# Kernel optimization log

Hardware: AMD Instinct MI355X
Metric: run time of the kernel (lower is better)

The kernel has to match this reference:

```python
import jax, jax.numpy as jnp
import numpy as np

B, S, E, H = 4, 2048, 1024, 16
DH = E // H
EXP = 1024  # FeedForwardPart default expansion_dim
EPS = 1e-5


def layer_norm(x, gamma, beta):
    mu = jnp.mean(x, axis=-1, keepdims=True)
    var = jnp.var(x, axis=-1, keepdims=True)
    return (x - mu) * jax.lax.rsqrt(var + EPS) * gamma + beta


def setup_inputs() -> dict:
    key = jax.random.key(0)
    ks = jax.random.split(key, 8)
    s = 0.02
    return {
        "x": jax.random.normal(ks[0], (B, S, E), jnp.float32),
        "mask": jnp.ones((B, 1, 1, S), jnp.int32),
        "wq": jax.random.normal(ks[1], (E, E), jnp.float32) * s,
        "wk": jax.random.normal(ks[2], (E, E), jnp.float32) * s,
        "wv": jax.random.normal(ks[3], (E, E), jnp.float32) * s,
        "wo": jax.random.normal(ks[4], (E, E), jnp.float32) * s,
        "bo": jnp.zeros((E,), jnp.float32),
        "w1": jax.random.normal(ks[5], (E, EXP), jnp.float32) * s,
        "b1": jnp.zeros((EXP,), jnp.float32),
        "w2": jax.random.normal(ks[6], (EXP, E), jnp.float32) * s,
        "b2": jnp.zeros((E,), jnp.float32),
        "gamma": jnp.ones((E,), jnp.float32),
        "beta": jnp.zeros((E,), jnp.float32),
    }


def reference(x, mask, wq, wk, wv, wo, bo, w1, b1, w2, b2, gamma, beta):
    # Multi-head self-attention
    q = (x @ wq).reshape(B, S, H, DH)
    k = (x @ wk).reshape(B, S, H, DH)
    v = (x @ wv).reshape(B, S, H, DH)
    scores = jnp.einsum("bqhd,bkhd->bhqk", q, k) / jnp.sqrt(jnp.float32(DH))
    scores = jnp.where(mask == 0, jnp.float32(-1e10), scores)
    attn = jax.nn.softmax(scores, axis=-1)
    ctx = jnp.einsum("bhqk,bkhd->bqhd", attn, v).reshape(B, S, E)
    attn_out = ctx @ wo + bo
    # Residual + shared LayerNorm
    h = layer_norm(attn_out + x, gamma, beta)
    # FFN (expansion 1024 per source default)
    ff = jax.nn.relu(h @ w1 + b1) @ w2 + b2
    return layer_norm(ff + h, gamma, beta)
```

## Files before the change

### kernel.cpp

```cpp
#include <hip/hip_runtime.h>
#include <hip/hip_bf16.h>

typedef short s16x8 __attribute__((ext_vector_type(8)));
typedef float f32x4 __attribute__((ext_vector_type(4)));
typedef float f32x16 __attribute__((ext_vector_type(16)));
typedef unsigned short u16;

#define B_ 4
#define S_ 2048
#define E_ 1024
#define H_ 16
#define DH_ 64

__device__ __forceinline__ u16 f2b(float f) {
  union { float f; unsigned u; } x; x.f = f;
  unsigned r = (x.u + 0x7fffu + ((x.u >> 16) & 1u)) >> 16;
  return (u16)r;
}

__device__ __forceinline__ float b2f(u16 v) {
  union { unsigned u; float f; } x; x.u = ((unsigned)v) << 16; return x.f;
}

__device__ __forceinline__ unsigned pk2(float lo, float hi) {
  __hip_bfloat162 h = __float22bfloat162_rn(float2{lo, hi});
  union { __hip_bfloat162 h; unsigned u; } c; c.h = h; return c.u;
}

__device__ __forceinline__ void xsw(unsigned& x, unsigned& y, int hi) {
  unsigned s = hi ? x : y;
  unsigned r = (unsigned)__shfl_xor((int)s, 32);
  unsigned nx = hi ? r : x;
  unsigned ny = hi ? y : r;
  x = nx; y = ny;
}

__device__ __forceinline__ void async16(const void* g, void* l) {
  __builtin_amdgcn_global_load_lds((const __attribute__((address_space(1))) void*)g,
                                   (__attribute__((address_space(3))) void*)l,
                                   16, 0, 0);
}

__global__ __launch_bounds__(256) void k_cast(const float* __restrict__ in,
                                              u16* __restrict__ out, int n4) {
  int i = blockIdx.x * 256 + threadIdx.x;
  if (i >= n4) return;
  float4 v = ((const float4*)in)[i];
  ushort4 o;
  o.x = f2b(v.x); o.y = f2b(v.y); o.z = f2b(v.z); o.w = f2b(v.w);
  ((ushort4*)out)[i] = o;
}

__global__ __launch_bounds__(256) void k_castT(const float* __restrict__ in,
                                               u16* __restrict__ out, int K, int N) {
  __shared__ float tile[32][33];
  int k0 = blockIdx.x * 32, n0 = blockIdx.y * 32;
  int tx = threadIdx.x, ty = threadIdx.y;
#pragma unroll
  for (int i = 0; i < 32; i += 8)
    tile[ty + i][tx] = in[(long)(k0 + ty + i) * N + n0 + tx];
  __syncthreads();
#pragma unroll
  for (int i = 0; i < 32; i += 8)
    out[(long)(n0 + ty + i) * K + k0 + tx] = f2b(tile[tx][ty + i]);
}

__global__ __launch_bounds__(256, 2) void k_gemm(
    const u16* __restrict__ A, const u16* __restrict__ Bt,
    int N, int K,
    const float* __restrict__ bias, int relu, int mode,
    float* __restrict__ outF, u16* __restrict__ outB,
    u16* __restrict__ oq, u16* __restrict__ ok, u16* __restrict__ ov) {
  __shared__ __align__(16) u16 Al[128 * 32];
  __shared__ __align__(16) u16 Bl[128 * 32];
  const int t = threadIdx.x;
  const int lane = t & 63, w = t >> 6;
  const int g = lane >> 4, li = lane & 15;
  const int wr = w >> 1, wc = w & 1;
  const int bm = blockIdx.x * 128, bn = blockIdx.y * 128;

  f32x4 acc[4][4] = {};

  const long ar0 = bm + (t >> 2), ar1 = bm + ((256 + t) >> 2);
  const long br0 = bn + (t >> 2), br1 = bn + ((256 + t) >> 2);
  const int c0 = (t & 3) * 8, c1 = ((256 + t) & 3) * 8;
  u16* aD0 = &Al[(w * 64) * 8];
  u16* aD1 = &Al[(256 + w * 64) * 8];
  u16* bD0 = &Bl[(w * 64) * 8];
  u16* bD1 = &Bl[(256 + w * 64) * 8];

  for (int kt = 0; kt < K; kt += 32) {
    async16(&A[ar0 * K + kt + c0], aD0);
    async16(&A[ar1 * K + kt + c1], aD1);
    async16(&Bt[br0 * K + kt + c0], bD0);
    async16(&Bt[br1 * K + kt + c1], bD1);
    __syncthreads();
    s16x8 af[4], bf[4];
#pragma unroll
    for (int mi = 0; mi < 4; ++mi)
      af[mi] = *(const s16x8*)&Al[(wr * 64 + mi * 16 + li) * 32 + g * 8];
#pragma unroll
    for (int nf = 0; nf < 4; ++nf)
      bf[nf] = *(const s16x8*)&Bl[(wc * 64 + nf * 16 + li) * 32 + g * 8];
#pragma unroll
    for (int mi = 0; mi < 4; ++mi)
#pragma unroll
      for (int nf = 0; nf < 4; ++nf)
        acc[mi][nf] = __builtin_amdgcn_mfma_f32_16x16x32_bf16(af[mi], bf[nf], acc[mi][nf], 0, 0, 0);
    __syncthreads();
  }

#pragma unroll
  for (int mi = 0; mi < 4; ++mi)
#pragma unroll
    for (int nf = 0; nf < 4; ++nf) {
      int col = bn + wc * 64 + nf * 16 + li;
      if (mode == 1) {
        int which = col >> 10, cc = col & 1023;
        int hh = cc >> 6, dd = cc & 63;
        u16* dst = which == 0 ? oq : (which == 1 ? ok : ov);
        float scl = which == 0 ? 0.125f : 1.f;
#pragma unroll
        for (int r = 0; r < 4; ++r) {
          long row = bm + wr * 64 + mi * 16 + g * 4 + r;
          int b2 = (int)(row >> 11), ss = (int)(row & 2047);
          dst[(((long)b2 * H_ + hh) * S_ + ss) * DH_ + dd] = f2b(acc[mi][nf][r] * scl);
        }
      } else {
        float bv = bias ? bias[col] : 0.f;
#pragma unroll
        for (int r = 0; r < 4; ++r) {
          long row = bm + wr * 64 + mi * 16 + g * 4 + r;
          float v = acc[mi][nf][r] + bv;
          if (relu) v = fmaxf(v, 0.f);
          if (outF) outF[row * N + col] = v;
          if (outB) outB[row * N + col] = f2b(v);
        }
      }
    }
}

__global__ __launch_bounds__(512, 1) void k_attn(
    const u16* __restrict__ Q, const u16* __restrict__ Kg, const u16* __restrict__ Vg,
    const int* __restrict__ mask, u16* __restrict__ ctx) {
  __shared__ __align__(16) u16 Kl[3][64 * 64];
  __shared__ __align__(16) u16 Vt[3][64 * 72];
  __shared__ __align__(16) float MBs[S_];
  __shared__ __align__(16) float BC[8 * 32];
  const int t = threadIdx.x;
  const int lane = t & 63, wid = t >> 6;
  const int q = lane & 31, hi = lane >> 5;
  const int bh = blockIdx.x;
  const int b = bh >> 4, h = bh & 15;
  const long bhoff = (long)bh * S_ * DH_;
  const int q0 = blockIdx.y * 256 + wid * 32;
  const int skey = t >> 3, sdj = t & 7;
  const int NT = S_ / 64;

  {
    int4 m4 = ((const int4*)(mask + (long)b * S_))[t];
    float4 f;
    f.x = m4.x ? 0.f : -1e10f; f.y = m4.y ? 0.f : -1e10f;
    f.z = m4.z ? 0.f : -1e10f; f.w = m4.w ? 0.f : -1e10f;
    ((float4*)MBs)[t] = f;
  }

  s16x8 qf[4];
  {
    const u16* Qp = Q + bhoff + (long)(q0 + q) * DH_;
#pragma unroll
    for (int c = 0; c < 4; ++c) qf[c] = *(const s16x8*)(Qp + c * 16 + hi * 8);
  }

  s16x8 kreg, vreg;
#define LOADKV(TI) { \
    kreg = *(const s16x8*)(Kg + bhoff + (long)((TI) * 64 + skey) * DH_ + sdj * 8); \
    vreg = *(const s16x8*)(Vg + bhoff + (long)((TI) * 64 + lane) * DH_ + wid * 8); }
#define WRITEKV(BUF) { \
    *(s16x8*)((char*)&Kl[BUF][0] + skey * 128 + ((sdj * 16) ^ ((skey & 7) << 4))) = kreg; \
    _Pragma("unroll") \
    for (int j = 0; j < 8; ++j) Vt[BUF][(wid * 8 + j) * 72 + lane] = (u16)vreg[j]; }

  const int swz = (q & 7) << 4;
#define QKSTEP(S0, S1, BUF) { \
    const char* Kc = (const char*)&Kl[BUF][0]; \
    _Pragma("unroll") \
    for (int c = 0; c < 4; ++c) { \
      s16x8 kf0 = *(const s16x8*)(Kc + q * 128 + ((c * 32 + hi * 16) ^ swz)); \
      s16x8 kf1 = *(const s16x8*)(Kc + (32 + q) * 128 + ((c * 32 + hi * 16) ^ swz)); \
      S0 = __builtin_amdgcn_mfma_f32_32x32x16_bf16(kf0, qf[c], S0, 0, 0, 0); \
      S1 = __builtin_amdgcn_mfma_f32_32x32x16_bf16(kf1, qf[c], S1, 0, 0, 0); \
    } }

#define SOFTPV(S0, S1, TI) { \
    const int kt = (TI) * 64; \
    const u16* Vc = &Vt[(TI) % 3][0]; \
    float p[32]; \
    float tmax = -1e30f; \
    _Pragma("unroll") \
    for (int g4 = 0; g4 < 4; ++g4) { \
      f32x4 mb0 = *(const f32x4*)&MBs[kt + g4 * 8 + hi * 4]; \
      f32x4 mb1 = *(const f32x4*)&MBs[kt + 32 + g4 * 8 + hi * 4]; \
      _Pragma("unroll") \
      for (int e = 0; e < 4; ++e) { \
        float v0 = S0[g4 * 4 + e] + mb0[e]; \
        float v1 = S1[g4 * 4 + e] + mb1[e]; \
        p[g4 * 4 + e] = v0; p[16 + g4 * 4 + e] = v1; \
        tmax = fmaxf(tmax, fmaxf(v0, v1)); \
      } \
    } \
    tmax = fmaxf(tmax, __shfl_xor(tmax, 32)); \
    if (!__all(tmax <= m_run + 8.f)) { \
      float mnew = fmaxf(m_run, tmax); \
      float corr = __expf(m_run - mnew); \
      m_run = mnew; l_run *= corr; \
      if (lane < 32) BC[wid * 32 + q] = corr; \
      asm volatile("s_waitcnt lgkmcnt(0)" ::: "memory"); \
      _Pragma("unroll") \
      for (int g4 = 0; g4 < 4; ++g4) { \
        f32x4 cv = *(const f32x4*)&BC[wid * 32 + g4 * 8 + hi * 4]; \
        _Pragma("unroll") \
        for (int e = 0; e < 4; ++e) { o0[g4 * 4 + e] *= cv[e]; o1[g4 * 4 + e] *= cv[e]; } \
      } \
    } \
    float ps = 0.f; \
    _Pragma("unroll") \
    for (int j = 0; j < 32; ++j) { float pv = __expf(p[j] - m_run); p[j] = pv; ps += pv; } \
    l_run += ps; \
    _Pragma("unroll") \
    for (int c = 0; c < 4; ++c) { \
      unsigned X1 = pk2(p[c * 8 + 0], p[c * 8 + 1]); \
      unsigned X2 = pk2(p[c * 8 + 2], p[c * 8 + 3]); \
      unsigned Y1 = pk2(p[c * 8 + 4], p[c * 8 + 5]); \
      unsigned Y2 = pk2(p[c * 8 + 6], p[c * 8 + 7]); \
      xsw(X1, Y1, hi); xsw(X2, Y2, hi); \
      union { unsigned u[4]; s16x8 v; } pu; \
      pu.u[0] = X1; pu.u[1] = X2; pu.u[2] = Y1; pu.u[3] = Y2; \
      s16x8 vb0 = *(const s16x8*)(Vc + (long)q * 72 + c * 16 + hi * 8); \
      s16x8 vb1 = *(const s16x8*)(Vc + (long)(32 + q) * 72 + c * 16 + hi * 8); \
      o0 = __builtin_amdgcn_mfma_f32_32x32x16_bf16(pu.v, vb0, o0, 0, 0, 0); \
      o1 = __builtin_amdgcn_mfma_f32_32x32x16_bf16(pu.v, vb1, o1, 0, 0, 0); \
    } }

#define ITER(I, SC0, SC1, SN0, SN1) { \
    const int ip1 = (I) + 1; \
    if (ip1 < NT) WRITEKV(ip1 % 3); \
    __syncthreads(); \
    if (ip1 < NT) { \
      SN0 = zz; SN1 = zz; \
      QKSTEP(SN0, SN1, ip1 % 3); \
      if (ip1 + 1 < NT) LOADKV(ip1 + 1); \
    } \
    SOFTPV(SC0, SC1, I); }

  f32x16 zz = {};
  f32x16 o0 = zz, o1 = zz;
  float m_run = -1e30f, l_run = 0.f;

  LOADKV(0);
  WRITEKV(0);
  __syncthreads();
  f32x16 sA0 = zz, sA1 = zz, sB0 = zz, sB1 = zz;
  QKSTEP(sA0, sA1, 0);
  LOADKV(1);

  for (int i = 0; i < NT; i += 2) {
    ITER(i, sA0, sA1, sB0, sB1);
    ITER(i + 1, sB0, sB1, sA0, sA1);
  }

  l_run += __shfl_xor(l_run, 32);
  float inv = 1.f / fmaxf(l_run, 1e-30f);
  if (lane < 32) BC[wid * 32 + q] = inv;
  asm volatile("s_waitcnt lgkmcnt(0)" ::: "memory");
#pragma unroll
  for (int g4 = 0; g4 < 4; ++g4) {
    f32x4 iv = *(const f32x4*)&BC[wid * 32 + g4 * 8 + hi * 4];
#pragma unroll
    for (int e = 0; e < 4; ++e) {
      int qr = e + g4 * 8 + hi * 4;
      long ro = ((long)(b * S_ + q0 + qr) * H_ + h) * DH_ + q;
      ctx[ro] = f2b(o0[g4 * 4 + e] * iv[e]);
      ctx[ro + 32] = f2b(o1[g4 * 4 + e] * iv[e]);
    }
  }
#undef LOADKV
#undef WRITEKV
#undef QKSTEP
#undef SOFTPV
#undef ITER
}

__global__ __launch_bounds__(256) void k_lnb(const u16* __restrict__ a, const u16* __restrict__ res,
                                             const float* __restrict__ gamma, const float* __restrict__ beta,
                                             float* __restrict__ outF, u16* __restrict__ outB) {
  const int row = blockIdx.x, t = threadIdx.x;
  const long base = (long)row * E_;
  ushort4 av = ((const ushort4*)(a + base))[t];
  ushort4 rv = ((const ushort4*)(res + base))[t];
  float4 s = make_float4(b2f(av.x) + b2f(rv.x), b2f(av.y) + b2f(rv.y),
                         b2f(av.z) + b2f(rv.z), b2f(av.w) + b2f(rv.w));
  float ps = s.x + s.y + s.z + s.w;
  float pq = s.x * s.x + s.y * s.y + s.z * s.z + s.w * s.w;
#pragma unroll
  for (int xm = 32; xm >= 1; xm >>= 1) { ps += __shfl_xor(ps, xm); pq += __shfl_xor(pq, xm); }
  __shared__ float red[8];
  int w = t >> 6, lane = t & 63;
  if (lane == 0) { red[w] = ps; red[4 + w] = pq; }
  __syncthreads();
  ps = red[0] + red[1] + red[2] + red[3];
  pq = red[4] + red[5] + red[6] + red[7];
  float mu = ps * (1.f / E_);
  float rs = rsqrtf(pq * (1.f / E_) - mu * mu + 1e-5f);
  float4 gv = ((const float4*)gamma)[t];
  float4 be = ((const float4*)beta)[t];
  float4 o = make_float4((s.x - mu) * rs * gv.x + be.x, (s.y - mu) * rs * gv.y + be.y,
                         (s.z - mu) * rs * gv.z + be.z, (s.w - mu) * rs * gv.w + be.w);
  if (outF) ((float4*)(outF + base))[t] = o;
  if (outB) {
    ushort4 ob; ob.x = f2b(o.x); ob.y = f2b(o.y); ob.z = f2b(o.z); ob.w = f2b(o.w);
    ((ushort4*)(outB + base))[t] = ob;
  }
}

extern "C" void kernel_launch(void* const* d_in, const int* in_sizes, int n_in,
                              void* d_out, int out_size, void* d_ws, size_t ws_size,
                              hipStream_t stream) {
  const float* x  = (const float*)d_in[0];
  const int* mask = (const int*)d_in[1];
  const float* wq = (const float*)d_in[2];
  const float* wk = (const float*)d_in[3];
  const float* wv = (const float*)d_in[4];
  const float* wo = (const float*)d_in[5];
  const float* bo = (const float*)d_in[6];
  const float* w1 = (const float*)d_in[7];
  const float* b1 = (const float*)d_in[8];
  const float* w2 = (const float*)d_in[9];
  const float* b2 = (const float*)d_in[10];
  const float* gamma = (const float*)d_in[11];
  const float* beta  = (const float*)d_in[12];
  float* out = (float*)d_out;

  char* ws = (char*)d_ws;
  const size_t MB = 1024ull * 1024ull;
  u16* xb  = (u16*)(ws + 0);
  u16* wqt = (u16*)(ws + 16 * MB);
  u16* wkt = (u16*)(ws + 18 * MB);
  u16* wvt = (u16*)(ws + 20 * MB);
  u16* wot = (u16*)(ws + 22 * MB);
  u16* w1t = (u16*)(ws + 24 * MB);
  u16* w2t = (u16*)(ws + 26 * MB);
  u16* qb  = (u16*)(ws + 28 * MB);
  u16* kb  = (u16*)(ws + 44 * MB);
  u16* vb  = (u16*)(ws + 60 * MB);
  u16* ctx = (u16*)(ws + 76 * MB);
  u16* aob = (u16*)(ws + 92 * MB);
  u16* hb  = (u16*)(ws + 108 * MB);
  u16* ff1 = qb;
  u16* ff2b = kb;

  const int n4 = B_ * S_ * E_ / 4;
  k_cast<<<n4 / 256, 256, 0, stream>>>(x, xb, n4);
  dim3 tg(E_ / 32, E_ / 32), tb(32, 8);
  k_castT<<<tg, tb, 0, stream>>>(wq, wqt, E_, E_);
  k_castT<<<tg, tb, 0, stream>>>(wk, wkt, E_, E_);
  k_castT<<<tg, tb, 0, stream>>>(wv, wvt, E_, E_);
  k_castT<<<tg, tb, 0, stream>>>(wo, wot, E_, E_);
  k_castT<<<tg, tb, 0, stream>>>(w1, w1t, E_, E_);
  k_castT<<<tg, tb, 0, stream>>>(w2, w2t, E_, E_);

  k_gemm<<<dim3(64, 24), 256, 0, stream>>>(xb, wqt, 3072, 1024, nullptr, 0, 1,
                                           nullptr, nullptr, qb, kb, vb);

  k_attn<<<dim3(B_ * H_, S_ / 256), 512, 0, stream>>>(qb, kb, vb, mask, ctx);

  dim3 gg(64, 8);
  k_gemm<<<gg, 256, 0, stream>>>(ctx, wot, 1024, 1024, bo, 0, 0, nullptr, aob,
                                 nullptr, nullptr, nullptr);
  k_lnb<<<B_ * S_, 256, 0, stream>>>(aob, xb, gamma, beta, nullptr, hb);
  k_gemm<<<gg, 256, 0, stream>>>(hb, w1t, 1024, 1024, b1, 1, 0, nullptr, ff1,
                                 nullptr, nullptr, nullptr);
  k_gemm<<<gg, 256, 0, stream>>>(ff1, w2t, 1024, 1024, b2, 0, 0, nullptr, ff2b,
                                 nullptr, nullptr, nullptr);
  k_lnb<<<B_ * S_, 256, 0, stream>>>(ff2b, hb, gamma, beta, out, nullptr);
}
```

Baseline: 330.4 us.

## Tune attention softmax with exp2 scaling, permlane swap, mask skip and priorities

Several changes to the attention kernel. The log2(e) factor is folded into the Q scale so the softmax can use exp2f, and the shuffle-based cross-half exchange is replaced with v_permlane32_swap. A per-64-key mask flag skips the mask-bias loads and adds when a tile is fully unmasked, and s_setprio is raised around the MFMA sections. Launch bounds are also loosened from 1 to 4 to permit higher occupancy, and the lazy-rescale threshold is widened to match the base-2 domain, which risks a larger range in the unnormalised accumulators.

```diff
diff --git a/kernel.cpp b/kernel.cpp
--- a/kernel.cpp
+++ b/kernel.cpp
@@ -27,12 +27,8 @@
   union { __hip_bfloat162 h; unsigned u; } c; c.h = h; return c.u;
 }
 
-__device__ __forceinline__ void xsw(unsigned& x, unsigned& y, int hi) {
-  unsigned s = hi ? x : y;
-  unsigned r = (unsigned)__shfl_xor((int)s, 32);
-  unsigned nx = hi ? r : x;
-  unsigned ny = hi ? y : r;
-  x = nx; y = ny;
+__device__ __forceinline__ void pl32swap(unsigned& x, unsigned& y) {
+  asm volatile("v_permlane32_swap_b32 %0, %1" : "+v"(x), "+v"(y));
 }
 
 __device__ __forceinline__ void async16(const void* g, void* l) {
@@ -119,7 +115,7 @@
         int which = col >> 10, cc = col & 1023;
         int hh = cc >> 6, dd = cc & 63;
         u16* dst = which == 0 ? oq : (which == 1 ? ok : ov);
-        float scl = which == 0 ? 0.125f : 1.f;
+        float scl = which == 0 ? 0.18033688011112042f : 1.f;
 #pragma unroll
         for (int r = 0; r < 4; ++r) {
           long row = bm + wr * 64 + mi * 16 + g * 4 + r;
@@ -140,12 +136,13 @@
     }
 }
 
-__global__ __launch_bounds__(512, 1) void k_attn(
+__global__ __launch_bounds__(512, 4) void k_attn(
     const u16* __restrict__ Q, const u16* __restrict__ Kg, const u16* __restrict__ Vg,
     const int* __restrict__ mask, u16* __restrict__ ctx) {
   __shared__ __align__(16) u16 Kl[3][64 * 64];
   __shared__ __align__(16) u16 Vt[3][64 * 72];
   __shared__ __align__(16) float MBs[S_];
+  __shared__ int MFlag[S_ / 64];
   __shared__ __align__(16) float BC[8 * 32];
   const int t = threadIdx.x;
   const int lane = t & 63, wid = t >> 6;
@@ -163,6 +160,10 @@
     f.x = m4.x ? 0.f : -1e10f; f.y = m4.y ? 0.f : -1e10f;
     f.z = m4.z ? 0.f : -1e10f; f.w = m4.w ? 0.f : -1e10f;
     ((float4*)MBs)[t] = f;
+    bool ok = m4.x && m4.y && m4.z && m4.w;
+    unsigned long long vote = __ballot(ok);
+    if ((lane & 15) == 0)
+      MFlag[t >> 4] = (((vote >> ((lane >> 4) * 16)) & 0xFFFFull) == 0xFFFFull);
   }
 
   s16x8 qf[4];
@@ -184,35 +185,47 @@
   const int swz = (q & 7) << 4;
 #define QKSTEP(S0, S1, BUF) { \
     const char* Kc = (const char*)&Kl[BUF][0]; \
+    __builtin_amdgcn_s_setprio(1); \
     _Pragma("unroll") \
     for (int c = 0; c < 4; ++c) { \
       s16x8 kf0 = *(const s16x8*)(Kc + q * 128 + ((c * 32 + hi * 16) ^ swz)); \
       s16x8 kf1 = *(const s16x8*)(Kc + (32 + q) * 128 + ((c * 32 + hi * 16) ^ swz)); \
       S0 = __builtin_amdgcn_mfma_f32_32x32x16_bf16(kf0, qf[c], S0, 0, 0, 0); \
       S1 = __builtin_amdgcn_mfma_f32_32x32x16_bf16(kf1, qf[c], S1, 0, 0, 0); \
-    } }
+    } \
+    __builtin_amdgcn_s_setprio(0); }
 
 #define SOFTPV(S0, S1, TI) { \
     const int kt = (TI) * 64; \
     const u16* Vc = &Vt[(TI) % 3][0]; \
+    const bool mok = MFlag[TI] != 0; \
     float p[32]; \
     float tmax = -1e30f; \
-    _Pragma("unroll") \
-    for (int g4 = 0; g4 < 4; ++g4) { \
-      f32x4 mb0 = *(const f32x4*)&MBs[kt + g4 * 8 + hi * 4]; \
-      f32x4 mb1 = *(const f32x4*)&MBs[kt + 32 + g4 * 8 + hi * 4]; \
+    if (mok) { \
       _Pragma("unroll") \
-      for (int e = 0; e < 4; ++e) { \
-        float v0 = S0[g4 * 4 + e] + mb0[e]; \
-        float v1 = S1[g4 * 4 + e] + mb1[e]; \
-        p[g4 * 4 + e] = v0; p[16 + g4 * 4 + e] = v1; \
+      for (int j = 0; j < 16; ++j) { \
+        float v0 = S0[j], v1 = S1[j]; \
+        p[j] = v0; p[16 + j] = v1; \
         tmax = fmaxf(tmax, fmaxf(v0, v1)); \
+      } \
+    } else { \
+      _Pragma("unroll") \
+      for (int g4 = 0; g4 < 4; ++g4) { \
+        f32x4 mb0 = *(const f32x4*)&MBs[kt + g4 * 8 + hi * 4]; \
+        f32x4 mb1 = *(const f32x4*)&MBs[kt + 32 + g4 * 8 + hi * 4]; \
+        _Pragma("unroll") \
+        for (int e = 0; e < 4; ++e) { \
+          float v0 = S0[g4 * 4 + e] + mb0[e]; \
+          float v1 = S1[g4 * 4 + e] + mb1[e]; \
+          p[g4 * 4 + e] = v0; p[16 + g4 * 4 + e] = v1; \
+          tmax = fmaxf(tmax, fmaxf(v0, v1)); \
+        } \
       } \
     } \
     tmax = fmaxf(tmax, __shfl_xor(tmax, 32)); \
-    if (!__all(tmax <= m_run + 8.f)) { \
+    if (!__all(tmax <= m_run + 11.5f)) { \
       float mnew = fmaxf(m_run, tmax); \
-      float corr = __expf(m_run - mnew); \
+      float corr = exp2f(m_run - mnew); \
       m_run = mnew; l_run *= corr; \
       if (lane < 32) BC[wid * 32 + q] = corr; \
       asm volatile("s_waitcnt lgkmcnt(0)" ::: "memory"); \
@@ -225,22 +238,24 @@
     } \
     float ps = 0.f; \
     _Pragma("unroll") \
-    for (int j = 0; j < 32; ++j) { float pv = __expf(p[j] - m_run); p[j] = pv; ps += pv; } \
+    for (int j = 0; j < 32; ++j) { float pv = exp2f(p[j] - m_run); p[j] = pv; ps += pv; } \
     l_run += ps; \
+    __builtin_amdgcn_s_setprio(1); \
     _Pragma("unroll") \
     for (int c = 0; c < 4; ++c) { \
       unsigned X1 = pk2(p[c * 8 + 0], p[c * 8 + 1]); \
       unsigned X2 = pk2(p[c * 8 + 2], p[c * 8 + 3]); \
       unsigned Y1 = pk2(p[c * 8 + 4], p[c * 8 + 5]); \
       unsigned Y2 = pk2(p[c * 8 + 6], p[c * 8 + 7]); \
-      xsw(X1, Y1, hi); xsw(X2, Y2, hi); \
+      pl32swap(X1, Y1); pl32swap(X2, Y2); \
       union { unsigned u[4]; s16x8 v; } pu; \
       pu.u[0] = X1; pu.u[1] = X2; pu.u[2] = Y1; pu.u[3] = Y2; \
       s16x8 vb0 = *(const s16x8*)(Vc + (long)q * 72 + c * 16 + hi * 8); \
       s16x8 vb1 = *(const s16x8*)(Vc + (long)(32 + q) * 72 + c * 16 + hi * 8); \
       o0 = __builtin_amdgcn_mfma_f32_32x32x16_bf16(pu.v, vb0, o0, 0, 0, 0); \
       o1 = __builtin_amdgcn_mfma_f32_32x32x16_bf16(pu.v, vb1, o1, 0, 0, 0); \
-    } }
+    } \
+    __builtin_amdgcn_s_setprio(0); }
 
 #define ITER(I, SC0, SC1, SN0, SN1) { \
     const int ip1 = (I) + 1; \
```

After: 744.7 us. 125% more time.
